# Kernel tuning notes

Measured on AMD Instinct MI355X. Metric: run time of the kernel, lower is better.

Reference implementation:

```python
import jax, jax.numpy as jnp
import numpy as np

NUM_HEADS = 16
EMBED_DIM = 1024

def setup_inputs() -> dict:
    key = jax.random.key(0)
    k1, k2, k3 = jax.random.split(key, 3)
    x = jax.random.normal(k1, (4, 2048, EMBED_DIM), dtype=jnp.float32)
    # Linear weights (lecun-style scaling for numerical sanity)
    w_qkv = jax.random.normal(k2, (EMBED_DIM, 3 * EMBED_DIM), dtype=jnp.float32) / np.sqrt(EMBED_DIM)
    w_out = jax.random.normal(k3, (EMBED_DIM, EMBED_DIM), dtype=jnp.float32) / np.sqrt(EMBED_DIM)
    return {"x": x, "w_qkv": w_qkv, "w_out": w_out}

def reference(x, w_qkv, w_out):
    b, s, d = x.shape
    h = NUM_HEADS
    dh = d // h
    qkv = x @ w_qkv                        # [b, s, 3d]
    q, k, v = jnp.split(qkv, 3, axis=-1)   # each [b, s, d]
    def split_heads(t):
        return t.reshape(b, s, h, dh).transpose(0, 2, 1, 3)  # [b, h, s, dh]
    q, k, v = split_heads(q), split_heads(k), split_heads(v)
    logits = jnp.einsum('bhsd,bhtd->bhst', q, k) / jnp.sqrt(jnp.asarray(dh, q.dtype))
    weights = jax.nn.softmax(logits, axis=-1)
    out = jnp.einsum('bhst,bhtd->bhsd', weights, v)
    out = out.transpose(0, 2, 1, 3).reshape(b, s, d)  # [b, s, d]
    return out @ w_out
```

## Files before the change

kernel.cpp:

```cpp
#include <hip/hip_runtime.h>
#include <hip/hip_bf16.h>
#include <math.h>

typedef unsigned short u16;
typedef unsigned long long u64;
typedef __attribute__((ext_vector_type(8))) short short8;
typedef __attribute__((ext_vector_type(4))) float floatx4;

#define BB 4
#define SS 2048
#define DD 1024
#define HH 16
#define DHH 64
#define BSZ (BB*SS)

__device__ inline u16 bf1(float f) {
  return (u16)((__float_as_uint(f) + 0x8000u) >> 16);
}
__device__ inline unsigned pk2bf(float a, float b) {
  return __builtin_amdgcn_perm(__float_as_uint(b) + 0x8000u,
                               __float_as_uint(a) + 0x8000u, 0x07060302u);
}

__device__ inline short8 ld16(const u16* p) {
  union { uint4 u; short8 s; } cv;
  cv.u = *(const uint4*)p;
  return cv.s;
}

__device__ inline void gload_lds16(const u16* g, u16* l) {
  __builtin_amdgcn_global_load_lds(
      (const __attribute__((address_space(1))) void*)g,
      (__attribute__((address_space(3))) void*)l, 16, 0, 0);
}

__global__ __launch_bounds__(256) void cvt_f32_bf16(
    const float* __restrict__ in, u16* __restrict__ out) {
  int t = blockIdx.x * 256 + threadIdx.x;
  const float4* p = (const float4*)in + (size_t)t * 2;
  float4 a = p[0], b = p[1];
  uint4 r;
  r.x = pk2bf(a.x, a.y); r.y = pk2bf(a.z, a.w);
  r.z = pk2bf(b.x, b.y); r.w = pk2bf(b.z, b.w);
  *((uint4*)out + t) = r;
}

__global__ __launch_bounds__(256) void transpose_f32_bf16(
    const float* __restrict__ in, u16* __restrict__ out, int K, int N) {
  __shared__ u16 tile[32][33];
  int k0 = blockIdx.y * 32, n0 = blockIdx.x * 32;
  int tx = threadIdx.x, ty = threadIdx.y;
  #pragma unroll
  for (int i = 0; i < 32; i += 8)
    tile[ty + i][tx] = bf1(in[(size_t)(k0 + ty + i) * N + n0 + tx]);
  __syncthreads();
  #pragma unroll
  for (int i = 0; i < 32; i += 8)
    out[(size_t)(n0 + ty + i) * K + k0 + tx] = tile[tx][ty + i];
}

template <int MODE>
__global__ __launch_bounds__(256) void gemm_nt(
    const u16* __restrict__ A, const u16* __restrict__ Bt,
    int M, int N, int K,
    float* __restrict__ outf, u16* __restrict__ q, u16* __restrict__ kk,
    u16* __restrict__ vv) {
  __shared__ __attribute__((aligned(16))) u16 As[128 * 32];
  __shared__ __attribute__((aligned(16))) u16 Bs[128 * 32];
  const int tid = threadIdx.x;
  const int lane = tid & 63;
  const int wave = tid >> 6;
  const int col = lane & 15, quad = lane >> 4;
  const int nbx = gridDim.x;
  const int nwg = nbx * gridDim.y;
  const int lin = blockIdx.y * nbx + blockIdx.x;
  const int swz = (lin & 7) * (nwg >> 3) + (lin >> 3);
  const int m0 = (swz / nbx) * 128, n0 = (swz % nbx) * 128;
  const int wm = (wave & 1) * 64, wn = (wave >> 1) * 64;

  floatx4 acc[4][4];
  #pragma unroll
  for (int i = 0; i < 4; i++)
    #pragma unroll
    for (int j = 0; j < 4; j++) acc[i][j] = (floatx4){0.f, 0.f, 0.f, 0.f};

  const u16* ga0 = A + (size_t)(m0 + (tid >> 2)) * K + (tid & 3) * 8;
  const u16* ga1 = ga0 + (size_t)64 * K;
  const u16* gb0 = Bt + (size_t)(n0 + (tid >> 2)) * K + (tid & 3) * 8;
  const u16* gb1 = gb0 + (size_t)64 * K;
  u16* lA0 = As + wave * 512;
  u16* lB0 = Bs + wave * 512;

  for (int kb = 0; kb < K; kb += 32) {
    __syncthreads();
    gload_lds16(ga0 + kb, lA0);
    gload_lds16(ga1 + kb, lA0 + 2048);
    gload_lds16(gb0 + kb, lB0);
    gload_lds16(gb1 + kb, lB0 + 2048);
    __syncthreads();
    short8 af[4], bfr[4];
    #pragma unroll
    for (int i = 0; i < 4; i++)
      af[i] = ld16(As + (wm + i * 16 + col) * 32 + quad * 8);
    #pragma unroll
    for (int i = 0; i < 4; i++)
      bfr[i] = ld16(Bs + (wn + i * 16 + col) * 32 + quad * 8);
    #pragma unroll
    for (int i = 0; i < 4; i++)
      #pragma unroll
      for (int j = 0; j < 4; j++)
        acc[i][j] = __builtin_amdgcn_mfma_f32_16x16x32_bf16(af[i], bfr[j],
                                                            acc[i][j], 0, 0, 0);
  }

  #pragma unroll
  for (int i = 0; i < 4; i++) {
    #pragma unroll
    for (int j = 0; j < 4; j++) {
      int gm0 = m0 + wm + i * 16 + quad * 4;
      int gn = n0 + wn + j * 16 + col;
      if (MODE == 0) {
        #pragma unroll
        for (int r = 0; r < 4; r++)
          outf[(size_t)(gm0 + r) * N + gn] = acc[i][j][r];
      } else {
        int which = gn >> 10;
        if (which == 2) {
          int dh = gn & 63, hh = (gn >> 6) & 15;
          int bb = gm0 >> 11, s = gm0 & 2047;
          uint2 pk;
          pk.x = pk2bf(acc[i][j][0], acc[i][j][1]);
          pk.y = pk2bf(acc[i][j][2], acc[i][j][3]);
          *(uint2*)(vv + ((size_t)((bb * HH + hh) * 64 + dh)) * SS + s) = pk;
        } else {
          int f = gn & 1023;
          u16* dst = (which == 0) ? q : kk;
          float sc = (which == 0) ? 0.18033688f : 1.0f;
          #pragma unroll
          for (int r = 0; r < 4; r++)
            dst[(size_t)(gm0 + r) * DD + f] = bf1(acc[i][j][r] * sc);
        }
      }
    }
  }
}

__global__ __launch_bounds__(256, 2) void attn_kernel(
    const u16* __restrict__ Q, const u16* __restrict__ K,
    const u16* __restrict__ VT, u16* __restrict__ O) {
  __shared__ __attribute__((aligned(16))) u16 Ks[64 * 72];
  __shared__ __attribute__((aligned(16))) u16 Vs[80 * 72];
  __shared__ __attribute__((aligned(16))) u16 Ps[4][64 * 72];

  const int tid = threadIdx.x, lane = tid & 63, wave = tid >> 6;
  const int col = lane & 15, quad = lane >> 4;
  const int bid = blockIdx.x;
  const int idx = ((bid & 7) << 6) + (bid >> 3);
  const int qt = idx & 7;
  const int h = (idx >> 3) & 15;
  const int b = idx >> 7;

  const size_t rowbase = (size_t)b * SS;
  const int qrow0 = qt * 256 + wave * 64;

  short8 qf[4][2];
  #pragma unroll
  for (int qs = 0; qs < 4; qs++)
    #pragma unroll
    for (int kc = 0; kc < 2; kc++)
      qf[qs][kc] = ld16(Q + (rowbase + qrow0 + qs * 16 + col) * DD + h * DHH +
                        kc * 32 + quad * 8);

  const u16* kg = K + rowbase * DD + h * DHH;
  const u16* vg = VT + (size_t)(b * HH + h) * DHH * SS;

  {
    int r = 64 + (tid >> 4), c = (tid & 15) * 4;
    u16 val = (r == 64) ? (u16)0x3F80 : (u16)0;
    Vs[r * 72 + c] = val; Vs[r * 72 + c + 1] = val;
    Vs[r * 72 + c + 2] = val; Vs[r * 72 + c + 3] = val;
  }

  floatx4 o[4][5];
  #pragma unroll
  for (int qs = 0; qs < 4; qs++)
    #pragma unroll
    for (int mt = 0; mt < 5; mt++) o[qs][mt] = (floatx4){0.f, 0.f, 0.f, 0.f};

  const int srow = tid >> 2, sc = (tid & 3) * 16;
  u16* pw = &Ps[wave][0];

  uint4 k0 = *(const uint4*)(kg + (size_t)srow * DD + sc);
  uint4 k1 = *(const uint4*)(kg + (size_t)srow * DD + sc + 8);
  uint4 v0 = *(const uint4*)(vg + (size_t)srow * SS + sc);
  uint4 v1 = *(const uint4*)(vg + (size_t)srow * SS + sc + 8);

  for (int kt = 0; kt < SS; kt += 64) {
    __syncthreads();
    *(uint4*)(Ks + srow * 72 + sc) = k0;
    *(uint4*)(Ks + srow * 72 + sc + 8) = k1;
    *(uint4*)(Vs + srow * 72 + sc) = v0;
    *(uint4*)(Vs + srow * 72 + sc + 8) = v1;
    __syncthreads();

    if (kt + 64 < SS) {
      k0 = *(const uint4*)(kg + (size_t)(kt + 64 + srow) * DD + sc);
      k1 = *(const uint4*)(kg + (size_t)(kt + 64 + srow) * DD + sc + 8);
      v0 = *(const uint4*)(vg + (size_t)srow * SS + kt + 64 + sc);
      v1 = *(const uint4*)(vg + (size_t)srow * SS + kt + 64 + sc + 8);
    }

    #pragma unroll
    for (int mt = 0; mt < 4; mt++) {
      short8 kf0 = ld16(Ks + (mt * 16 + col) * 72 + quad * 8);
      short8 kf1 = ld16(Ks + (mt * 16 + col) * 72 + 32 + quad * 8);
      #pragma unroll
      for (int qs = 0; qs < 4; qs++) {
        floatx4 s = (floatx4){0.f, 0.f, 0.f, 0.f};
        s = __builtin_amdgcn_mfma_f32_16x16x32_bf16(kf0, qf[qs][0], s, 0, 0, 0);
        s = __builtin_amdgcn_mfma_f32_16x16x32_bf16(kf1, qf[qs][1], s, 0, 0, 0);
        uint2 pk;
        pk.x = pk2bf(__builtin_amdgcn_exp2f(s[0]), __builtin_amdgcn_exp2f(s[1]));
        pk.y = pk2bf(__builtin_amdgcn_exp2f(s[2]), __builtin_amdgcn_exp2f(s[3]));
        *(uint2*)(pw + (qs * 16 + col) * 72 + mt * 16 + quad * 4) = pk;
      }
    }

    short8 a[5][2];
    #pragma unroll
    for (int mt = 0; mt < 5; mt++)
      #pragma unroll
      for (int kc = 0; kc < 2; kc++)
        a[mt][kc] = ld16(Vs + (mt * 16 + col) * 72 + kc * 32 + quad * 8);
    #pragma unroll
    for (int qs = 0; qs < 4; qs++) {
      short8 b0 = ld16(pw + (qs * 16 + col) * 72 + quad * 8);
      short8 b1 = ld16(pw + (qs * 16 + col) * 72 + 32 + quad * 8);
      #pragma unroll
      for (int mt = 0; mt < 5; mt++) {
        o[qs][mt] =
            __builtin_amdgcn_mfma_f32_16x16x32_bf16(a[mt][0], b0, o[qs][mt], 0, 0, 0);
        o[qs][mt] =
            __builtin_amdgcn_mfma_f32_16x16x32_bf16(a[mt][1], b1, o[qs][mt], 0, 0, 0);
      }
    }
  }

  #pragma unroll
  for (int qs = 0; qs < 4; qs++) {
    float l = __shfl(o[qs][4][0], col, 64);
    float inv = 1.0f / l;
    u16* ob = O + (rowbase + qrow0 + qs * 16 + col) * DD + h * DHH;
    #pragma unroll
    for (int mt = 0; mt < 4; mt++) {
      uint2 pk;
      pk.x = pk2bf(o[qs][mt][0] * inv, o[qs][mt][1] * inv);
      pk.y = pk2bf(o[qs][mt][2] * inv, o[qs][mt][3] * inv);
      *(uint2*)(ob + mt * 16 + quad * 4) = pk;
    }
  }
}

extern "C" void kernel_launch(void* const* d_in, const int* in_sizes, int n_in,
                              void* d_out, int out_size, void* d_ws,
                              size_t ws_size, hipStream_t stream) {
  const float* x = (const float*)d_in[0];
  const float* w_qkv = (const float*)d_in[1];
  const float* w_out = (const float*)d_in[2];
  float* out = (float*)d_out;

  u16* ws = (u16*)d_ws;
  u16* wT = ws;
  u16* q = wT + (size_t)3072 * 1024;
  u16* vt = q + (size_t)BSZ * DD;
  u16* k = (u16*)d_out;
  u16* xb = k + (size_t)BSZ * DD;
  u16* att = q;

  cvt_f32_bf16<<<dim3(BSZ * DD / (256 * 8)), 256, 0, stream>>>(x, xb);
  transpose_f32_bf16<<<dim3(3072 / 32, 1024 / 32), dim3(32, 8), 0, stream>>>(
      w_qkv, wT, 1024, 3072);
  gemm_nt<1><<<dim3(3072 / 128, BSZ / 128), 256, 0, stream>>>(
      xb, wT, BSZ, 3072, 1024, nullptr, q, k, vt);
  transpose_f32_bf16<<<dim3(1024 / 32, 1024 / 32), dim3(32, 8), 0, stream>>>(
      w_out, wT, 1024, 1024);
  attn_kernel<<<dim3(BB * HH * (SS / 256)), 256, 0, stream>>>(q, k, vt, att);
  gemm_nt<0><<<dim3(1024 / 128, BSZ / 128), 256, 0, stream>>>(
      att, wT, BSZ, 1024, 1024, out, nullptr, nullptr, nullptr);
}
```

Baseline: 278.8 us.

## Keep softmax probabilities in registers via permlane swaps instead of LDS round-trip

```diff
diff --git a/kernel.cpp b/kernel.cpp
--- a/kernel.cpp
+++ b/kernel.cpp
@@ -32,6 +32,11 @@
   __builtin_amdgcn_global_load_lds(
       (const __attribute__((address_space(1))) void*)g,
       (__attribute__((address_space(3))) void*)l, 16, 0, 0);
+}
+
+__device__ inline void swap_qpair(unsigned &a, unsigned &b) {
+  asm("v_permlane32_swap_b32 %0, %1" : "+v"(a), "+v"(b));
+  asm("v_permlane16_swap_b32 %0, %1" : "+v"(a), "+v"(b));
 }
 
 __global__ __launch_bounds__(256) void cvt_f32_bf16(
@@ -150,7 +155,6 @@
     const u16* __restrict__ VT, u16* __restrict__ O) {
   __shared__ __attribute__((aligned(16))) u16 Ks[64 * 72];
   __shared__ __attribute__((aligned(16))) u16 Vs[80 * 72];
-  __shared__ __attribute__((aligned(16))) u16 Ps[4][64 * 72];
 
   const int tid = threadIdx.x, lane = tid & 63, wave = tid >> 6;
   const int col = lane & 15, quad = lane >> 4;
@@ -188,7 +192,6 @@
     for (int mt = 0; mt < 5; mt++) o[qs][mt] = (floatx4){0.f, 0.f, 0.f, 0.f};
 
   const int srow = tid >> 2, sc = (tid & 3) * 16;
-  u16* pw = &Ps[wave][0];
 
   uint4 k0 = *(const uint4*)(kg + (size_t)srow * DD + sc);
   uint4 k1 = *(const uint4*)(kg + (size_t)srow * DD + sc + 8);
@@ -211,37 +214,40 @@
     }
 
     #pragma unroll
-    for (int mt = 0; mt < 4; mt++) {
-      short8 kf0 = ld16(Ks + (mt * 16 + col) * 72 + quad * 8);
-      short8 kf1 = ld16(Ks + (mt * 16 + col) * 72 + 32 + quad * 8);
+    for (int h2 = 0; h2 < 2; h2++) {
+      unsigned pk[4][2][2];
+      #pragma unroll
+      for (int mtl = 0; mtl < 2; mtl++) {
+        const int mt = h2 * 2 + mtl;
+        short8 kf0 = ld16(Ks + (mt * 16 + col) * 72 + quad * 8);
+        short8 kf1 = ld16(Ks + (mt * 16 + col) * 72 + 32 + quad * 8);
+        #pragma unroll
+        for (int qs = 0; qs < 4; qs++) {
+          floatx4 s = (floatx4){0.f, 0.f, 0.f, 0.f};
+          s = __builtin_amdgcn_mfma_f32_16x16x32_bf16(kf0, qf[qs][0], s, 0, 0, 0);
+          s = __builtin_amdgcn_mfma_f32_16x16x32_bf16(kf1, qf[qs][1], s, 0, 0, 0);
+          pk[qs][mtl][0] =
+              pk2bf(__builtin_amdgcn_exp2f(s[0]), __builtin_amdgcn_exp2f(s[1]));
+          pk[qs][mtl][1] =
+              pk2bf(__builtin_amdgcn_exp2f(s[2]), __builtin_amdgcn_exp2f(s[3]));
+        }
+      }
+      short8 va[5];
+      #pragma unroll
+      for (int mt5 = 0; mt5 < 5; mt5++)
+        va[mt5] = ld16(Vs + (mt5 * 16 + col) * 72 + h2 * 32 + quad * 8);
       #pragma unroll
       for (int qs = 0; qs < 4; qs++) {
-        floatx4 s = (floatx4){0.f, 0.f, 0.f, 0.f};
-        s = __builtin_amdgcn_mfma_f32_16x16x32_bf16(kf0, qf[qs][0], s, 0, 0, 0);
-        s = __builtin_amdgcn_mfma_f32_16x16x32_bf16(kf1, qf[qs][1], s, 0, 0, 0);
-        uint2 pk;
-        pk.x = pk2bf(__builtin_amdgcn_exp2f(s[0]), __builtin_amdgcn_exp2f(s[1]));
-        pk.y = pk2bf(__builtin_amdgcn_exp2f(s[2]), __builtin_amdgcn_exp2f(s[3]));
-        *(uint2*)(pw + (qs * 16 + col) * 72 + mt * 16 + quad * 4) = pk;
-      }
-    }
-
-    short8 a[5][2];
-    #pragma unroll
-    for (int mt = 0; mt < 5; mt++)
-      #pragma unroll
-      for (int kc = 0; kc < 2; kc++)
-        a[mt][kc] = ld16(Vs + (mt * 16 + col) * 72 + kc * 32 + quad * 8);
-    #pragma unroll
-    for (int qs = 0; qs < 4; qs++) {
-      short8 b0 = ld16(pw + (qs * 16 + col) * 72 + quad * 8);
-      short8 b1 = ld16(pw + (qs * 16 + col) * 72 + 32 + quad * 8);
-      #pragma unroll
-      for (int mt = 0; mt < 5; mt++) {
-        o[qs][mt] =
-            __builtin_amdgcn_mfma_f32_16x16x32_bf16(a[mt][0], b0, o[qs][mt], 0, 0, 0);
-        o[qs][mt] =
-            __builtin_amdgcn_mfma_f32_16x16x32_bf16(a[mt][1], b1, o[qs][mt], 0, 0, 0);
+        unsigned wa = pk[qs][0][0], wb = pk[qs][1][0];
+        swap_qpair(wa, wb);
+        unsigned wc = pk[qs][0][1], wd = pk[qs][1][1];
+        swap_qpair(wc, wd);
+        union { unsigned u[4]; short8 s8; } bb;
+        bb.u[0] = wa; bb.u[1] = wc; bb.u[2] = wb; bb.u[3] = wd;
+        #pragma unroll
+        for (int mt5 = 0; mt5 < 5; mt5++)
+          o[qs][mt5] = __builtin_amdgcn_mfma_f32_16x16x32_bf16(
+              va[mt5], bb.s8, o[qs][mt5], 0, 0, 0);
       }
     }
   }
```

After: 267.9 us. 1.04x faster.
